# Optimization experiments

Measured on AMD Instinct MI355X. Metric: run time of the kernel, lower is better.

The kernel has to match this reference:

```python
import jax, jax.numpy as jnp
import numpy as np

H, B, N, D, VD, FFH = 8, 16, 512, 512, 64, 2048
NPICK = N // 2
NORM = 1.0 / np.sqrt(VD)


def _ha_encoder(h, W_query, W_key, W_val, W1, W2, W3, W4, W5, W6):
    # h: [B, N, D]; weights: [H, D, VD]
    np_ = NPICK
    pick, dlv = h[:, :np_], h[:, np_:]
    proj = lambda x, W: jnp.einsum('bnd,hdk->hbnk', x, W)
    Q, K, V = proj(h, W_query), proj(h, W_key), proj(h, W_val)
    Kp, Kd = K[:, :, :np_], K[:, :, np_:]   # shared projections (same W_key)
    Vp, Vd = V[:, :, :np_], V[:, :, np_:]
    Qp = proj(pick, W1); Qpap = proj(pick, W2); Qpad = proj(pick, W3)
    Qd = proj(dlv, W4);  Qdad = proj(dlv, W5);  Qdap = proj(dlv, W6)
    c_main = NORM * jnp.einsum('hbnk,hbmk->hbnm', Q, K)          # [H,B,N,N]
    c_pd = NORM * jnp.sum(Qp * Kd, -1)                           # [H,B,np] paired pick->delivery
    c_pap = NORM * jnp.einsum('hbnk,hbmk->hbnm', Qpap, Kp)       # pick -> all pick
    c_pad = NORM * jnp.einsum('hbnk,hbmk->hbnm', Qpad, Kd)       # pick -> all delivery
    c_dp = NORM * jnp.sum(Qd * Kp, -1)                           # paired delivery->pick
    c_dad = NORM * jnp.einsum('hbnk,hbmk->hbnm', Qdad, Kd)       # delivery -> all delivery
    c_dap = NORM * jnp.einsum('hbnk,hbmk->hbnm', Qdap, Kp)       # delivery -> all pick
    ninf1 = jnp.full((H, h.shape[0], np_), -jnp.inf, c_main.dtype)
    ninf2 = jnp.full((H, h.shape[0], np_, np_), -jnp.inf, c_main.dtype)
    col_pd = jnp.concatenate([c_pd, ninf1], 2)[..., None]        # [H,B,N,1]
    blk_pap = jnp.concatenate([c_pap, ninf2], 2)                 # [H,B,N,np]
    blk_pad = jnp.concatenate([c_pad, ninf2], 2)
    col_dp = jnp.concatenate([ninf1, c_dp], 2)[..., None]
    blk_dad = jnp.concatenate([ninf2, c_dad], 2)
    blk_dap = jnp.concatenate([ninf2, c_dap], 2)
    compat = jnp.concatenate([c_main, col_pd, blk_pap, blk_pad, col_dp, blk_dad, blk_dap], -1)
    a = jax.nn.softmax(compat, -1)                               # [H,B,N,N+2+4*np]
    zpad = jnp.zeros_like(Vd)
    V_add_d = jnp.concatenate([Vd, zpad], 2)                     # [H,B,N,VD]
    V_add_p = jnp.concatenate([zpad, Vp], 2)
    av = lambda w, v: jnp.einsum('hbnm,hbmv->hbnv', w, v)
    i = N
    heads = av(a[..., :N], V)
    heads = heads + a[..., i:i + 1] * V_add_d; i += 1
    heads = heads + av(a[..., i:i + np_], Vp); i += np_
    heads = heads + av(a[..., i:i + np_], Vd); i += np_
    heads = heads + a[..., i:i + 1] * V_add_p; i += 1
    heads = heads + av(a[..., i:i + np_], Vd); i += np_
    heads = heads + av(a[..., i:i + np_], Vp)
    return heads.transpose(1, 2, 0, 3).reshape(h.shape[0], N, H * VD)


def _split_heads(x):
    b, n, hd = x.shape
    return x.reshape(b, n, H, hd // H).transpose(0, 2, 1, 3)


def _mha(q, k, v):
    dk = q.shape[-1]
    w = jax.nn.softmax(jnp.einsum('bhnd,bhmd->bhnm', q, k) / np.sqrt(dk), -1)
    o = jnp.einsum('bhnm,bhmd->bhnd', w, v)
    b, hh, n, d = o.shape
    return o.transpose(0, 2, 1, 3).reshape(b, n, hh * d)


def _ff(x, w1, b1, w2, b2, a):
    return x + (jax.nn.relu(x @ w1 + b1) @ w2 + b2) * a


def _forward(x, W_query, W_key, W_val, W1_query, W2_query, W3_query, W4_query, W5_query, W6_query,
             Wq_w, Wk_w, Wv_w, Wq2p_w, Wq2d_w, Wk2_w, Wv2_w,
             comb_w, comb_b, comb2_w, comb2_b, comb3_w, comb3_b,
             alpha1, alpha2, alpha3,
             ff1_w1, ff1_b1, ff1_w2, ff1_b2, ffa1,
             ff2_w1, ff2_b1, ff2_w2, ff2_b2, ffa2,
             ff3_w1, ff3_b1, ff3_w2, ff3_b2, ffa3):
    # stage 1: heterogeneous attention block (combine_3 / AN3 / FF3)
    ha = _ha_encoder(x, W_query, W_key, W_val, W1_query, W2_query, W3_query, W4_query, W5_query, W6_query)
    out = x + (ha @ comb3_w + comb3_b) * alpha3
    out = _ff(out, ff3_w1, ff3_b1, ff3_w2, ff3_b2, ffa3)
    # stage 2: standard multi-head self-attention (combine / AN1 / FF1)
    q = _split_heads(out @ Wq_w); k = _split_heads(out @ Wk_w); v = _split_heads(out @ Wv_w)
    out = out + (_mha(q, k, v) @ comb_w + comb_b) * alpha1
    out = _ff(out, ff1_w1, ff1_b1, ff1_w2, ff1_b2, ffa1)
    # stage 3: pickup/delivery specific queries (combine_2 / AN2 / FF2)
    q2 = jnp.concatenate([out[:, :NPICK] @ Wq2p_w, out[:, NPICK:] @ Wq2d_w], 1)
    q2 = _split_heads(q2); k2 = _split_heads(out @ Wk2_w); v2 = _split_heads(out @ Wv2_w)
    out = out + (_mha(q2, k2, v2) @ comb2_w + comb2_b) * alpha2
    out = _ff(out, ff2_w1, ff2_b1, ff2_w2, ff2_b2, ffa2)
    return out


def setup_inputs() -> dict:
    key = jax.random.key(0)
    ks = jax.random.split(key, 64)
    it = iter(range(64))
    def nrm(shape):
        return jax.random.normal(ks[next(it)], shape, jnp.float32)
    def uni(shape):
        s = 1.0 / np.sqrt(shape[-1])  # torch init_parameters: uniform(-1/sqrt(size(-1)), ...)
        return jax.random.uniform(ks[next(it)], shape, jnp.float32, -s, s)
    d = {'x': nrm((B, N, D))}
    for n in ['W_query', 'W_key', 'W_val', 'W1_query', 'W2_query', 'W3_query', 'W4_query', 'W5_query', 'W6_query']:
        d[n] = uni((H, D, VD))
    for n in ['Wq_w', 'Wk_w', 'Wv_w', 'Wq2p_w', 'Wq2d_w', 'Wk2_w', 'Wv2_w']:
        d[n] = uni((D, H * VD))
    for n in ['comb_w', 'comb2_w', 'comb3_w']:
        d[n] = uni((H * VD, D))
    for n in ['comb_b', 'comb2_b', 'comb3_b']:
        d[n] = uni((D,))
    for n in ['alpha1', 'alpha2', 'alpha3']:
        d[n] = uni((1,))
    for i in ['1', '2', '3']:
        d['ff' + i + '_w1'] = uni((D, FFH))
        d['ff' + i + '_b1'] = uni((FFH,))
        d['ff' + i + '_w2'] = uni((FFH, D))
        d['ff' + i + '_b2'] = uni((D,))
        d['ffa' + i] = uni((1,))
    return d


def reference(x, W_query, W_key, W_val, W1_query, W2_query, W3_query, W4_query, W5_query, W6_query,
              Wq_w, Wk_w, Wv_w, Wq2p_w, Wq2d_w, Wk2_w, Wv2_w,
              comb_w, comb_b, comb2_w, comb2_b, comb3_w, comb3_b,
              alpha1, alpha2, alpha3,
              ff1_w1, ff1_b1, ff1_w2, ff1_b2, ffa1,
              ff2_w1, ff2_b1, ff2_w2, ff2_b2, ffa2,
              ff3_w1, ff3_b1, ff3_w2, ff3_b2, ffa3):
    return _forward(x, W_query, W_key, W_val, W1_query, W2_query, W3_query, W4_query, W5_query, W6_query,
                    Wq_w, Wk_w, Wv_w, Wq2p_w, Wq2d_w, Wk2_w, Wv2_w,
                    comb_w, comb_b, comb2_w, comb2_b, comb3_w, comb3_b,
                    alpha1, alpha2, alpha3,
                    ff1_w1, ff1_b1, ff1_w2, ff1_b2, ffa1,
                    ff2_w1, ff2_b1, ff2_w2, ff2_b2, ffa2,
                    ff3_w1, ff3_b1, ff3_w2, ff3_b2, ffa3)
```

## Files before the change

kernel.cpp:

```cpp
#include <hip/hip_runtime.h>
#include <math.h>

#define Hh 8
#define Bb 16
#define Nn 512
#define Dd 512
#define VDd 64
#define NPICKk 256
#define NORMF 0.125f
#define SCL2 0.1803368801f

typedef unsigned short ushortT;
typedef __bf16 bf16x8 __attribute__((ext_vector_type(8)));
typedef float f32x4 __attribute__((ext_vector_type(4)));

struct PtrsB { const ushortT* p[12]; };
struct PtrsD { ushortT* p[6]; };
struct Ptrs9 { const float* p[9]; };
struct Ptrs10 { const float* p[10]; };
struct Ptrs6 { const float* p[6]; };

__device__ inline ushortT f2bf(float f) {
    __bf16 h = (__bf16)f;
    union { __bf16 h; ushortT u; } v; v.h = h;
    return v.u;
}
__device__ inline float bf2f(ushortT u) {
    union { unsigned int u; float f; } v; v.u = ((unsigned int)u) << 16;
    return v.f;
}
__device__ inline float exp2fast(float x) {
#if __has_builtin(__builtin_amdgcn_exp2f)
    return __builtin_amdgcn_exp2f(x);
#else
    return exp2f(x);
#endif
}
__device__ inline void gload16(const void* gptr, void* ldsptr) {
    auto g = reinterpret_cast<const __attribute__((address_space(1))) unsigned int*>(
        reinterpret_cast<uintptr_t>(gptr));
    auto l = reinterpret_cast<__attribute__((address_space(3))) unsigned int*>(
        reinterpret_cast<uintptr_t>(ldsptr));
    __builtin_amdgcn_global_load_lds(g, l, 16, 0, 0);
}

#define LIX(r, g) (((r) << 6) + ((((g) ^ ((r) & 7))) << 3))

__global__ __launch_bounds__(256) void castx(const float* __restrict__ in,
                                             ushortT* __restrict__ out) {
    int i = blockIdx.x * 256 + threadIdx.x;
    float4 v = *(const float4*)&in[(size_t)i * 4];
    ushort4 o; o.x = f2bf(v.x); o.y = f2bf(v.y); o.z = f2bf(v.z); o.w = f2bf(v.w);
    *(ushort4*)&out[(size_t)i * 4] = o;
}

__device__ inline void tbody(const float* __restrict__ in, ushortT* __restrict__ out,
                             int in_ld, int out_ld, int r0, int c0) {
    __shared__ float T[64][65];
    int tr = threadIdx.x >> 4, tc4 = (threadIdx.x & 15) * 4;
#pragma unroll
    for (int p = 0; p < 4; ++p) {
        float4 v = *(const float4*)&in[(size_t)(r0 + tr + p * 16) * in_ld + c0 + tc4];
        T[tr + p * 16][tc4 + 0] = v.x; T[tr + p * 16][tc4 + 1] = v.y;
        T[tr + p * 16][tc4 + 2] = v.z; T[tr + p * 16][tc4 + 3] = v.w;
    }
    __syncthreads();
#pragma unroll
    for (int p = 0; p < 4; ++p) {
        int orow = c0 + tr + p * 16;
        int ocol = r0 + tc4;
        ushort4 o;
        o.x = f2bf(T[tc4 + 0][tr + p * 16]);
        o.y = f2bf(T[tc4 + 1][tr + p * 16]);
        o.z = f2bf(T[tc4 + 2][tr + p * 16]);
        o.w = f2bf(T[tc4 + 3][tr + p * 16]);
        *(ushort4*)&out[(size_t)orow * out_ld + ocol] = o;
    }
}

__global__ __launch_bounds__(256) void thead(Ptrs9 s, ushortT* __restrict__ dst) {
    int w = blockIdx.z >> 3, h = blockIdx.z & 7;
    tbody(s.p[w] + (size_t)h * 512 * 64,
          dst + (size_t)w * 262144 + (size_t)h * 64 * 512,
          64, 512, blockIdx.y * 64, 0);
}
__global__ __launch_bounds__(256) void tsq(Ptrs10 s, ushortT* __restrict__ dst) {
    tbody(s.p[blockIdx.z], dst + (size_t)blockIdx.z * 262144,
          512, 512, blockIdx.y * 64, blockIdx.x * 64);
}
__global__ __launch_bounds__(256) void tff(Ptrs6 s, ushortT* __restrict__ dst) {
    int z = blockIdx.z;
    if (z < 3) { if (blockIdx.y >= 8 || blockIdx.x >= 32) return; }
    else       { if (blockIdx.y >= 32 || blockIdx.x >= 8) return; }
    int in_ld = (z < 3) ? 2048 : 512;
    int out_ld = (z < 3) ? 512 : 2048;
    tbody(s.p[z], dst + (size_t)z * 1048576, in_ld, out_ld,
          blockIdx.y * 64, blockIdx.x * 64);
}

__global__ __launch_bounds__(256) void gemm_bf(
    PtrsB Bp, PtrsD Db, const ushortT* __restrict__ A, float* __restrict__ outF,
    int M, int N, int K, const float* __restrict__ bias,
    const float* __restrict__ res, const float* __restrict__ alpha,
    int do_relu, int nroute, int vtmask, int scmask)
{
    __shared__ __align__(16) ushortT As[128 * 64];
    __shared__ __align__(16) ushortT Bs[128 * 64];
    const int tid = threadIdx.x;
    const int wid = tid >> 6, lane = tid & 63;
    const int wm = wid >> 1, wn = wid & 1;
    const int l15 = lane & 15, l4 = lane >> 4;

    int bid = blockIdx.y * gridDim.x + blockIdx.x;
    int nwg = gridDim.x * gridDim.y;
    int q = nwg >> 3;
    int swz = (bid & 7) * q + (bid >> 3);
    int bx = swz % gridDim.x, by = swz / gridDim.x;

    const int r0 = by * 128, c0 = bx * 128;
    const int half = ((r0 & (Nn - 1)) >= NPICKk) ? 1 : 0;
    const ushortT* Bt = Bp.p[((c0 >> 9) << 1) | half];
    const int cB = nroute ? (c0 & 511) : c0;

    const ushortT* aSrc[4];
    const ushortT* bSrc[4];
    char* ldsA[4];
    char* ldsB[4];
#pragma unroll
    for (int i = 0; i < 4; ++i) {
        int off = wid * 4096 + i * 1024 + lane * 16;
        int row = off >> 7;
        int sg = ((off >> 4) & 7) ^ (row & 7);
        aSrc[i] = A + (size_t)(r0 + row) * K + sg * 8;
        bSrc[i] = Bt + (size_t)(cB + row) * K + sg * 8;
        ldsA[i] = (char*)As + off;
        ldsB[i] = (char*)Bs + off;
    }

    f32x4 acc[4][4] = {};

    for (int kt = 0; kt < K; kt += 64) {
        __syncthreads();
#pragma unroll
        for (int i = 0; i < 4; ++i) {
            gload16(aSrc[i] + kt, ldsA[i]);
            gload16(bSrc[i] + kt, ldsB[i]);
        }
        asm volatile("s_waitcnt vmcnt(0)" ::: "memory");
        __syncthreads();
#pragma unroll
        for (int kk = 0; kk < 2; ++kk) {
            int g0 = kk * 4 + l4;
            bf16x8 af[4], bfv[4];
#pragma unroll
            for (int mi = 0; mi < 4; ++mi)
                af[mi] = *(const bf16x8*)&As[LIX(wm * 64 + mi * 16 + l15, g0)];
#pragma unroll
            for (int ni = 0; ni < 4; ++ni)
                bfv[ni] = *(const bf16x8*)&Bs[LIX(wn * 64 + ni * 16 + l15, g0)];
#pragma unroll
            for (int mi = 0; mi < 4; ++mi)
#pragma unroll
                for (int ni = 0; ni < 4; ++ni)
                    acc[mi][ni] = __builtin_amdgcn_mfma_f32_16x16x32_bf16(
                        bfv[ni], af[mi], acc[mi][ni], 0, 0, 0);
        }
    }

    if (nroute) {
#pragma unroll
        for (int mi = 0; mi < 4; ++mi) {
            int row = r0 + wm * 64 + mi * 16 + l15;
#pragma unroll
            for (int ni = 0; ni < 4; ++ni) {
                int col = c0 + wn * 64 + ni * 16 + l4 * 4;
                int range = col >> 9, cc = col & 511;
                ushortT* d = Db.p[range];
                f32x4 a = acc[mi][ni];
                if ((scmask >> range) & 1) {
                    a[0] *= SCL2; a[1] *= SCL2; a[2] *= SCL2; a[3] *= SCL2;
                }
                if ((vtmask >> range) & 1) {
                    size_t vb = ((size_t)(row >> 9) * Hh + (cc >> 6)) * 64 + (cc & 63);
                    int tok = row & 511;
#pragma unroll
                    for (int r = 0; r < 4; ++r)
                        d[((vb + r) << 9) + tok] = f2bf(a[r]);
                } else {
                    ushort4 o;
                    o.x = f2bf(a[0]); o.y = f2bf(a[1]);
                    o.z = f2bf(a[2]); o.w = f2bf(a[3]);
                    *(ushort4*)&d[((size_t)row << 9) + cc] = o;
                }
            }
        }
    } else {
        const float alp = alpha ? alpha[0] : 1.0f;
        ushortT* outB = Db.p[0];
#pragma unroll
        for (int mi = 0; mi < 4; ++mi) {
            int row = r0 + wm * 64 + mi * 16 + l15;
#pragma unroll
            for (int ni = 0; ni < 4; ++ni) {
                int colb = c0 + wn * 64 + ni * 16 + l4 * 4;
                f32x4 a = acc[mi][ni];
                if (bias) {
                    float4 b4 = *(const float4*)&bias[colb];
                    a[0] += b4.x; a[1] += b4.y; a[2] += b4.z; a[3] += b4.w;
                }
                if (do_relu) {
#pragma unroll
                    for (int r = 0; r < 4; ++r) a[r] = fmaxf(a[r], 0.f);
                }
#pragma unroll
                for (int r = 0; r < 4; ++r) a[r] *= alp;
                size_t idx = (size_t)row * N + colb;
                if (res) {
                    float4 r4 = *(const float4*)&res[idx];
                    a[0] += r4.x; a[1] += r4.y; a[2] += r4.z; a[3] += r4.w;
                }
                if (outF)
                    *(float4*)&outF[idx] = make_float4(a[0], a[1], a[2], a[3]);
                if (outB) {
                    ushort4 o;
                    o.x = f2bf(a[0]); o.y = f2bf(a[1]);
                    o.z = f2bf(a[2]); o.w = f2bf(a[3]);
                    *(ushort4*)&outB[idx] = o;
                }
            }
        }
    }
}

__global__ __launch_bounds__(256) void gemm64(
    const ushortT* __restrict__ Bw, const ushortT* __restrict__ A,
    float* __restrict__ outF, ushortT* __restrict__ outB,
    int M, int N, int K, const float* __restrict__ bias,
    const float* __restrict__ resf, const ushortT* __restrict__ resb,
    const float* __restrict__ alpha, int do_relu)
{
    __shared__ __align__(16) ushortT As[64 * 64];
    __shared__ __align__(16) ushortT Bs[128 * 64];
    const int tid = threadIdx.x;
    const int wid = tid >> 6, lane = tid & 63;
    const int wm = wid >> 1, wn = wid & 1;
    const int l15 = lane & 15, l4 = lane >> 4;

    int bid = blockIdx.y * gridDim.x + blockIdx.x;
    int nwg = gridDim.x * gridDim.y;
    int q = nwg >> 3;
    int swz = (bid & 7) * q + (bid >> 3);
    int bx = swz % gridDim.x, by = swz / gridDim.x;
    const int r0 = by * 64, c0 = bx * 128;

    const ushortT* aSrc[2];
    char* ldsA[2];
#pragma unroll
    for (int i = 0; i < 2; ++i) {
        int off = wid * 2048 + i * 1024 + lane * 16;
        int row = off >> 7;
        int sg = ((off >> 4) & 7) ^ (row & 7);
        aSrc[i] = A + (size_t)(r0 + row) * K + sg * 8;
        ldsA[i] = (char*)As + off;
    }
    const ushortT* bSrc[4];
    char* ldsB[4];
#pragma unroll
    for (int i = 0; i < 4; ++i) {
        int off = wid * 4096 + i * 1024 + lane * 16;
        int row = off >> 7;
        int sg = ((off >> 4) & 7) ^ (row & 7);
        bSrc[i] = Bw + (size_t)(c0 + row) * K + sg * 8;
        ldsB[i] = (char*)Bs + off;
    }

    f32x4 acc[2][4] = {};

    for (int kt = 0; kt < K; kt += 64) {
        __syncthreads();
#pragma unroll
        for (int i = 0; i < 2; ++i) gload16(aSrc[i] + kt, ldsA[i]);
#pragma unroll
        for (int i = 0; i < 4; ++i) gload16(bSrc[i] + kt, ldsB[i]);
        asm volatile("s_waitcnt vmcnt(0)" ::: "memory");
        __syncthreads();
#pragma unroll
        for (int kk = 0; kk < 2; ++kk) {
            int g0 = kk * 4 + l4;
            bf16x8 af[2], bfv[4];
#pragma unroll
            for (int mi = 0; mi < 2; ++mi)
                af[mi] = *(const bf16x8*)&As[LIX(wm * 32 + mi * 16 + l15, g0)];
#pragma unroll
            for (int ni = 0; ni < 4; ++ni)
                bfv[ni] = *(const bf16x8*)&Bs[LIX(wn * 64 + ni * 16 + l15, g0)];
#pragma unroll
            for (int mi = 0; mi < 2; ++mi)
#pragma unroll
                for (int ni = 0; ni < 4; ++ni)
                    acc[mi][ni] = __builtin_amdgcn_mfma_f32_16x16x32_bf16(
                        bfv[ni], af[mi], acc[mi][ni], 0, 0, 0);
        }
    }

    const float alp = alpha ? alpha[0] : 1.0f;
#pragma unroll
    for (int mi = 0; mi < 2; ++mi) {
        int row = r0 + wm * 32 + mi * 16 + l15;
#pragma unroll
        for (int ni = 0; ni < 4; ++ni) {
            int colb = c0 + wn * 64 + ni * 16 + l4 * 4;
            f32x4 a = acc[mi][ni];
            if (bias) {
                float4 b4 = *(const float4*)&bias[colb];
                a[0] += b4.x; a[1] += b4.y; a[2] += b4.z; a[3] += b4.w;
            }
            if (do_relu) {
#pragma unroll
                for (int r = 0; r < 4; ++r) a[r] = fmaxf(a[r], 0.f);
            }
#pragma unroll
            for (int r = 0; r < 4; ++r) a[r] *= alp;
            size_t idx = (size_t)row * N + colb;
            if (resf) {
                float4 r4 = *(const float4*)&resf[idx];
                a[0] += r4.x; a[1] += r4.y; a[2] += r4.z; a[3] += r4.w;
            }
            if (resb) {
                ushort4 r4 = *(const ushort4*)&resb[idx];
                a[0] += bf2f(r4.x); a[1] += bf2f(r4.y);
                a[2] += bf2f(r4.z); a[3] += bf2f(r4.w);
            }
            if (outF)
                *(float4*)&outF[idx] = make_float4(a[0], a[1], a[2], a[3]);
            if (outB) {
                ushort4 o;
                o.x = f2bf(a[0]); o.y = f2bf(a[1]);
                o.z = f2bf(a[2]); o.w = f2bf(a[3]);
                *(ushort4*)&outB[idx] = o;
            }
        }
    }
}

__global__ __launch_bounds__(256) void diag_dot_bb(const ushortT* __restrict__ QD,
                                                   const ushortT* __restrict__ K,
                                                   float* __restrict__ Sdg) {
    int i = blockIdx.x * 256 + threadIdx.x;
    int h = i & 7, n = (i >> 3) & 511, b = i >> 12;
    int dix = (n < NPICKk) ? n + NPICKk : n - NPICKk;
    const ushortT* q = QD + (((size_t)(b * Nn + n) * Hh + h) << 6);
    const ushortT* k = K + (((size_t)(b * Nn + dix) * Hh + h) << 6);
    float s = 0.f;
#pragma unroll
    for (int d = 0; d < 64; d += 4) {
        ushort4 a = *(const ushort4*)(q + d);
        ushort4 c = *(const ushort4*)(k + d);
        s += bf2f(a.x) * bf2f(c.x) + bf2f(a.y) * bf2f(c.y)
           + bf2f(a.z) * bf2f(c.z) + bf2f(a.w) * bf2f(c.w);
    }
    Sdg[i] = s;
}

template <int HA>
__global__ __launch_bounds__(256) void attn9(
    const ushortT* __restrict__ Qm, const ushortT* __restrict__ Km,
    const ushortT* __restrict__ Vtm, const ushortT* __restrict__ QAm,
    const ushortT* __restrict__ QBm, const float* __restrict__ Sdg,
    ushortT* __restrict__ Out)
{
    __shared__ __align__(16) ushortT Ks[64 * 64];
    __shared__ __align__(16) ushortT Vs[64 * 64];
    __shared__ __align__(16) ushortT Pw[4][16 * 64];
    __shared__ float sdl[64];

    const int tid = threadIdx.x, wid = tid >> 6, lane = tid & 63;
    const int l15 = lane & 15, l4 = lane >> 4;

    const int p = blockIdx.x + (blockIdx.y << 3) + (blockIdx.z << 6);
    const int n0 = (((p >> 3) & 7)) << 6;
    const int g8 = (p & 7) | ((p >> 6) << 3);
    const int h = g8 & 7, b = g8 >> 3;
    const int bh = b * Hh + h;

    const size_t qrow = (((size_t)(b * Nn + n0 + wid * 16 + l15) * Hh + h) << 6);
    bf16x8 qf[2], xaf[2], xbf[2];
#pragma unroll
    for (int kk = 0; kk < 2; ++kk) {
        int g0 = kk * 4 + l4;
        qf[kk] = *(const bf16x8*)&Qm[qrow + g0 * 8];
        if (HA) {
            xaf[kk] = *(const bf16x8*)&QAm[qrow + g0 * 8];
            xbf[kk] = *(const bf16x8*)&QBm[qrow + g0 * 8];
        }
    }
    if (HA && tid < 64) sdl[tid] = Sdg[((size_t)(b * Nn + n0 + tid)) * Hh + h];
    const int td = (n0 < NPICKk) ? ((n0 + NPICKk) >> 6) : ((n0 - NPICKk) >> 6);

    const ushortT* kSrc[2]; char* kDst[2];
    const ushortT* vSrc[2]; char* vDst[2];
#pragma unroll
    for (int i = 0; i < 2; ++i) {
        int off = wid * 2048 + i * 1024 + lane * 16;
        int row = off >> 7, sg = ((off >> 4) & 7) ^ (row & 7);
        kSrc[i] = Km + (((size_t)(b * Nn + row) * Hh + h) << 6) + sg * 8;
        kDst[i] = (char*)Ks + off;
        vSrc[i] = Vtm + (((size_t)(bh * 64 + row)) << 9) + sg * 8;
        vDst[i] = (char*)Vs + off;
    }

    float M[4], L[4];
    f32x4 Oa[4] = {};
#pragma unroll
    for (int r = 0; r < 4; ++r) { M[r] = -INFINITY; L[r] = 0.f; }

    for (int t = 0; t < 8; ++t) {
        __syncthreads();
#pragma unroll
        for (int i = 0; i < 2; ++i) {
            gload16(kSrc[i] + (size_t)t * (64 * Hh * VDd), kDst[i]);
            gload16(vSrc[i] + t * 64, vDst[i]);
        }
        asm volatile("s_waitcnt vmcnt(0)" ::: "memory");
        __syncthreads();

        __builtin_amdgcn_s_setprio(1);
        f32x4 s1[4] = {}, sX[4] = {};
#pragma unroll
        for (int kk = 0; kk < 2; ++kk) {
            bf16x8 aq = qf[kk];
            bf16x8 ax;
            if (HA) ax = (t >= 4) ? xbf[kk] : xaf[kk];
#pragma unroll
            for (int ni = 0; ni < 4; ++ni) {
                bf16x8 bk = *(const bf16x8*)&Ks[LIX(ni * 16 + l15, kk * 4 + l4)];
                s1[ni] = __builtin_amdgcn_mfma_f32_16x16x32_bf16(aq, bk, s1[ni], 0, 0, 0);
                if (HA)
                    sX[ni] = __builtin_amdgcn_mfma_f32_16x16x32_bf16(ax, bk, sX[ni], 0, 0, 0);
            }
        }
        __builtin_amdgcn_s_setprio(0);

        const bool dt = HA && (t == td);

        float mrow[4];
        bool need = false;
#pragma unroll
        for (int r = 0; r < 4; ++r) {
            int rw = wid * 16 + l4 * 4 + r;
            float m = s1[0][r];
#pragma unroll
            for (int ni = 1; ni < 4; ++ni) m = fmaxf(m, s1[ni][r]);
            if (HA) {
#pragma unroll
                for (int ni = 0; ni < 4; ++ni) m = fmaxf(m, sX[ni][r]);
            }
            if (dt) m = fmaxf(m, sdl[rw]);
#pragma unroll
            for (int o = 8; o >= 1; o >>= 1) m = fmaxf(m, __shfl_xor(m, o, 16));
            mrow[r] = m;
            need = need || (m > M[r] + 8.f);
        }
        if (__any(need)) {
#pragma unroll
            for (int r = 0; r < 4; ++r) {
                float mn = fmaxf(M[r], mrow[r]);
                float sc = exp2fast(M[r] - mn);
                M[r] = mn; L[r] *= sc;
#pragma unroll
                for (int ni = 0; ni < 4; ++ni) Oa[ni][r] *= sc;
            }
        }

#pragma unroll
        for (int r = 0; r < 4; ++r) {
            int rw = wid * 16 + l4 * 4 + r;
            float rs = 0.f;
#pragma unroll
            for (int ni = 0; ni < 4; ++ni) {
                float pv = exp2fast(s1[ni][r] - M[r]);
                if (HA) pv += exp2fast(sX[ni][r] - M[r]);
                if (dt && ni == wid && l15 == l4 * 4 + r) pv += exp2fast(sdl[rw] - M[r]);
                s1[ni][r] = pv;
                rs += pv;
            }
#pragma unroll
            for (int o = 8; o >= 1; o >>= 1) rs += __shfl_xor(rs, o, 16);
            L[r] += rs;
        }

#pragma unroll
        for (int ni = 0; ni < 4; ++ni)
#pragma unroll
            for (int r = 0; r < 4; ++r) {
                int prow = l4 * 4 + r;
                int col = ni * 16 + l15;
                Pw[wid][(prow << 6) + ((((col >> 3) ^ (prow & 7))) << 3) + (col & 7)] =
                    f2bf(s1[ni][r]);
            }

        __builtin_amdgcn_s_setprio(1);
#pragma unroll
        for (int kk = 0; kk < 2; ++kk) {
            int g0 = kk * 4 + l4;
            bf16x8 ap = *(const bf16x8*)&Pw[wid][LIX(l15, g0)];
#pragma unroll
            for (int ni = 0; ni < 4; ++ni) {
                bf16x8 bv = *(const bf16x8*)&Vs[LIX(ni * 16 + l15, g0)];
                Oa[ni] = __builtin_amdgcn_mfma_f32_16x16x32_bf16(ap, bv, Oa[ni], 0, 0, 0);
            }
        }
        __builtin_amdgcn_s_setprio(0);
    }

#pragma unroll
    for (int r = 0; r < 4; ++r) {
        float inv = 1.0f / L[r];
        size_t obase = (((size_t)(b * Nn + n0 + wid * 16 + l4 * 4 + r) * Hh + h) << 6);
#pragma unroll
        for (int ni = 0; ni < 4; ++ni)
            Out[obase + ni * 16 + l15] = f2bf(Oa[ni][r] * inv);
    }
}

extern "C" void kernel_launch(void* const* d_in, const int* in_sizes, int n_in,
                              void* d_out, int out_size, void* d_ws, size_t ws_size,
                              hipStream_t stream)
{
    const float* x = (const float*)d_in[0];

    int dictOrder = (in_sizes[18] != 512);
    const float* comb_w  = (const float*)d_in[17];
    const float* comb2_w = (const float*)d_in[dictOrder ? 18 : 19];
    const float* comb3_w = (const float*)d_in[dictOrder ? 19 : 21];
    const float* comb_b  = (const float*)d_in[dictOrder ? 20 : 18];
    const float* comb2_b = (const float*)d_in[dictOrder ? 21 : 20];
    const float* comb3_b = (const float*)d_in[22];
    const float* alpha1 = (const float*)d_in[23];
    const float* alpha2 = (const float*)d_in[24];
    const float* alpha3 = (const float*)d_in[25];
    const float* ff1_w1 = (const float*)d_in[26];
    const float* ff1_b1 = (const float*)d_in[27];
    const float* ff1_w2 = (const float*)d_in[28];
    const float* ff1_b2 = (const float*)d_in[29];
    const float* ffa1   = (const float*)d_in[30];
    const float* ff2_w1 = (const float*)d_in[31];
    const float* ff2_b1 = (const float*)d_in[32];
    const float* ff2_w2 = (const float*)d_in[33];
    const float* ff2_b2 = (const float*)d_in[34];
    const float* ffa2   = (const float*)d_in[35];
    const float* ff3_w1 = (const float*)d_in[36];
    const float* ff3_b1 = (const float*)d_in[37];
    const float* ff3_w2 = (const float*)d_in[38];
    const float* ff3_b2 = (const float*)d_in[39];
    const float* ffa3   = (const float*)d_in[40];

    char* W = (char*)d_ws;
    ushortT* wbHead = (ushortT*)(W + 0);
    ushortT* wbMha  = (ushortT*)(W + 4718592);
    ushortT* wbComb = (ushortT*)(W + 8388608);
    ushortT* wbFf1  = (ushortT*)(W + 9961472);
    ushortT* wbFf2  = (ushortT*)(W + 16252928);
    ushortT* xbf    = (ushortT*)(W + 22544384);
    float*   Sd     = (float*)  (W + 30932992);
    ushortT* bufQ   = (ushortT*)(W + 31195136);
    ushortT* bufK   = (ushortT*)(W + 39583744);
    ushortT* bufVt  = (ushortT*)(W + 47972352);
    ushortT* bufQA  = (ushortT*)(W + 56360960);
    ushortT* bufQB  = (ushortT*)(W + 64749568);
    ushortT* bufQD  = (ushortT*)(W + 73138176);
    ushortT* hidden = (ushortT*)(W + 81526784);
    ushortT* curb   = (ushortT*)(W + 115081216);
    ushortT* bufHA  = xbf;
    float*   cur    = (float*)d_out;

    dim3 tb(256);
    const int TOK = Bb * Nn;
    const size_t WS = 512 * 512;
    const size_t WF = 2048 * 512;

    hipLaunchKernelGGL(castx, dim3(TOK * 512 / 1024), tb, 0, stream, x, xbf);
    {
        Ptrs9 s; for (int i = 0; i < 9; ++i) s.p[i] = (const float*)d_in[1 + i];
        hipLaunchKernelGGL(thead, dim3(1, 8, 72), tb, 0, stream, s, wbHead);
    }
    {
        Ptrs10 s;
        for (int i = 0; i < 7; ++i) s.p[i] = (const float*)d_in[10 + i];
        s.p[7] = comb_w; s.p[8] = comb2_w; s.p[9] = comb3_w;
        hipLaunchKernelGGL(tsq, dim3(8, 8, 10), tb, 0, stream, s, wbMha);
    }
    {
        Ptrs6 s;
        s.p[0] = ff1_w1; s.p[1] = ff2_w1; s.p[2] = ff3_w1;
        s.p[3] = ff1_w2; s.p[4] = ff2_w2; s.p[5] = ff3_w2;
        hipLaunchKernelGGL(tff, dim3(32, 32, 6), tb, 0, stream, s, wbFf1);
    }

    auto gemm = [&](PtrsB Bp, PtrsD Db, const ushortT* A, float* oF,
                    int M, int Ncc, int Kc, const float* bias, const float* res,
                    const float* alp, int relu, int nroute, int vtmask, int scmask) {
        hipLaunchKernelGGL(gemm_bf, dim3(Ncc / 128, M / 128), tb, 0, stream,
                           Bp, Db, A, oF, M, Ncc, Kc, bias, res, alp, relu, nroute,
                           vtmask, scmask);
    };
    auto g64 = [&](const ushortT* Bw, const ushortT* A, float* oF, ushortT* oB,
                   int M, int Ncc, int Kc, const float* bias, const float* resf,
                   const ushortT* resb, const float* alp, int relu) {
        hipLaunchKernelGGL(gemm64, dim3(Ncc / 128, M / 64), tb, 0, stream,
                           Bw, A, oF, oB, M, Ncc, Kc, bias, resf, resb, alp, relu);
    };
    auto uni = [&](const ushortT* w) { PtrsB b; for (int i = 0; i < 12; ++i) b.p[i] = w; return b; };
    auto d1 = [&](ushortT* d) { PtrsD dd = {}; dd.p[0] = d; return dd; };

    {
        PtrsB b;
        b.p[0] = b.p[1] = wbHead + 0 * WS;
        b.p[2] = b.p[3] = wbHead + 1 * WS;
        b.p[4] = b.p[5] = wbHead + 2 * WS;
        b.p[6] = wbHead + 4 * WS; b.p[7] = wbHead + 8 * WS;
        b.p[8] = wbHead + 5 * WS; b.p[9] = wbHead + 7 * WS;
        b.p[10] = wbHead + 3 * WS; b.p[11] = wbHead + 6 * WS;
        PtrsD d; d.p[0] = bufQ; d.p[1] = bufK; d.p[2] = bufVt;
        d.p[3] = bufQA; d.p[4] = bufQB; d.p[5] = bufQD;
        gemm(b, d, xbf, nullptr, TOK, 3072, 512, nullptr, nullptr, nullptr, 0, 6, 4, 57);
    }

    hipLaunchKernelGGL(diag_dot_bb, dim3(Bb * Nn * Hh / 256), tb, 0, stream, bufQD, bufK, Sd);
    hipLaunchKernelGGL((attn9<1>), dim3(Nn / 64, Hh, Bb), tb, 0, stream,
                       bufQ, bufK, bufVt, bufQA, bufQB, Sd, bufHA);

    g64(wbComb + 2 * WS, bufHA, nullptr, curb, TOK, 512, 512, comb3_b, x, nullptr, alpha3, 0);
    gemm(uni(wbFf1 + 2 * WF), d1(hidden), curb, nullptr, TOK, 2048, 512, ff3_b1, nullptr, nullptr, 1, 0, 0, 0);
    g64(wbFf2 + 2 * WF, hidden, nullptr, curb, TOK, 512, 2048, ff3_b2, nullptr, curb, ffa3, 0);

    {
        PtrsB b;
        b.p[0] = b.p[1] = wbMha + 0 * WS;
        b.p[2] = b.p[3] = wbMha + 1 * WS;
        b.p[4] = b.p[5] = wbMha + 2 * WS;
        PtrsD d = {}; d.p[0] = bufQ; d.p[1] = bufK; d.p[2] = bufVt;
        gemm(b, d, curb, nullptr, TOK, 1536, 512, nullptr, nullptr, nullptr, 0, 3, 4, 1);
    }
    hipLaunchKernelGGL((attn9<0>), dim3(Nn / 64, Hh, Bb), tb, 0, stream,
                       bufQ, bufK, bufVt, nullptr, nullptr, nullptr, bufHA);
    g64(wbComb + 0 * WS, bufHA, nullptr, curb, TOK, 512, 512, comb_b, nullptr, curb, alpha1, 0);
    gemm(uni(wbFf1 + 0 * WF), d1(hidden), curb, nullptr, TOK, 2048, 512, ff1_b1, nullptr, nullptr, 1, 0, 0, 0);
    g64(wbFf2 + 0 * WF, hidden, nullptr, curb, TOK, 512, 2048, ff1_b2, nullptr, curb, ffa1, 0);

    {
        PtrsB b;
        b.p[0] = wbMha + 3 * WS; b.p[1] = wbMha + 4 * WS;
        b.p[2] = b.p[3] = wbMha + 5 * WS;
        b.p[4] = b.p[5] = wbMha + 6 * WS;
        PtrsD d = {}; d.p[0] = bufQ; d.p[1] = bufK; d.p[2] = bufVt;
        gemm(b, d, curb, nullptr, TOK, 1536, 512, nullptr, nullptr, nullptr, 0, 3, 4, 1);
    }
    hipLaunchKernelGGL((attn9<0>), dim3(Nn / 64, Hh, Bb), tb, 0, stream,
                       bufQ, bufK, bufVt, nullptr, nullptr, nullptr, bufHA);
    g64(wbComb + 1 * WS, bufHA, nullptr, curb, TOK, 512, 512, comb2_b, nullptr, curb, alpha2, 0);
    gemm(uni(wbFf1 + 1 * WF), d1(hidden), curb, nullptr, TOK, 2048, 512, ff2_b1, nullptr, nullptr, 1, 0, 0, 0);
    g64(wbFf2 + 1 * WF, hidden, cur, nullptr, TOK, 512, 2048, ff2_b2, nullptr, curb, ffa2, 0);
}
```

Measured before the change: 502.4 us.

## Register-prefetch next K/V tile in attention and defer row-sum reduction

The attention kernel now loads the next K/V tile from global memory into registers while the current tile is computed, then stores it to shared memory at the top of the next iteration, replacing synchronous direct-to-LDS loads with a full vmcnt wait. The per-tile max shuffle reduction is moved inside the rare rescale branch, and the row-sum shuffle reduction is deferred to the epilogue using per-lane partial sums. Both aim to hide global load latency and cut cross-lane shuffles per tile. The cost is more registers for the prefetch buffers, which may reduce occupancy. The skip test for rescaling now compares per-lane maxima instead of the reduced row maximum.

```diff
diff --git a/kernel.cpp b/kernel.cpp
--- a/kernel.cpp
+++ b/kernel.cpp
@@ -363,7 +363,7 @@
 }
 
 template <int HA>
-__global__ __launch_bounds__(256) void attn9(
+__global__ __launch_bounds__(256) void attn10(
     const ushortT* __restrict__ Qm, const ushortT* __restrict__ Km,
     const ushortT* __restrict__ Vtm, const ushortT* __restrict__ QAm,
     const ushortT* __restrict__ QBm, const float* __restrict__ Sdg,
@@ -397,32 +397,49 @@
     if (HA && tid < 64) sdl[tid] = Sdg[((size_t)(b * Nn + n0 + tid)) * Hh + h];
     const int td = (n0 < NPICKk) ? ((n0 + NPICKk) >> 6) : ((n0 - NPICKk) >> 6);
 
-    const ushortT* kSrc[2]; char* kDst[2];
-    const ushortT* vSrc[2]; char* vDst[2];
+    const ushortT* kSrc[2]; ushortT* kDst[2];
+    const ushortT* vSrc[2]; ushortT* vDst[2];
 #pragma unroll
     for (int i = 0; i < 2; ++i) {
         int off = wid * 2048 + i * 1024 + lane * 16;
         int row = off >> 7, sg = ((off >> 4) & 7) ^ (row & 7);
         kSrc[i] = Km + (((size_t)(b * Nn + row) * Hh + h) << 6) + sg * 8;
-        kDst[i] = (char*)Ks + off;
+        kDst[i] = (ushortT*)((char*)Ks + off);
         vSrc[i] = Vtm + (((size_t)(bh * 64 + row)) << 9) + sg * 8;
-        vDst[i] = (char*)Vs + off;
-    }
-
-    float M[4], L[4];
+        vDst[i] = (ushortT*)((char*)Vs + off);
+    }
+
+    float M[4], Lp[4];
     f32x4 Oa[4] = {};
 #pragma unroll
-    for (int r = 0; r < 4; ++r) { M[r] = -INFINITY; L[r] = 0.f; }
-
+    for (int r = 0; r < 4; ++r) { M[r] = -INFINITY; Lp[r] = 0.f; }
+
+    bf16x8 krbuf[2][2], vrbuf[2][2];
+#pragma unroll
+    for (int i = 0; i < 2; ++i) {
+        krbuf[0][i] = *(const bf16x8*)kSrc[i];
+        vrbuf[0][i] = *(const bf16x8*)vSrc[i];
+    }
+
+#pragma unroll
     for (int t = 0; t < 8; ++t) {
-        __syncthreads();
+        const int cur = t & 1, nxt = cur ^ 1;
+        __builtin_amdgcn_s_barrier();
 #pragma unroll
         for (int i = 0; i < 2; ++i) {
-            gload16(kSrc[i] + (size_t)t * (64 * Hh * VDd), kDst[i]);
-            gload16(vSrc[i] + t * 64, vDst[i]);
-        }
-        asm volatile("s_waitcnt vmcnt(0)" ::: "memory");
-        __syncthreads();
+            *(bf16x8*)kDst[i] = krbuf[cur][i];
+            *(bf16x8*)vDst[i] = vrbuf[cur][i];
+        }
+        if (t < 7) {
+#pragma unroll
+            for (int i = 0; i < 2; ++i) {
+                krbuf[nxt][i] = *(const bf16x8*)(kSrc[i] + (size_t)(t + 1) * (64 * Hh * VDd));
+                vrbuf[nxt][i] = *(const bf16x8*)(vSrc[i] + (t + 1) * 64);
+            }
+        }
+        asm volatile("s_waitcnt lgkmcnt(0)" ::: "memory");
+        __builtin_amdgcn_s_barrier();
+        __builtin_amdgcn_sched_barrier(0);
 
         __builtin_amdgcn_s_setprio(1);
         f32x4 s1[4] = {}, sX[4] = {};
@@ -443,8 +460,8 @@
 
         const bool dt = HA && (t == td);
 
-        float mrow[4];
-        bool need = false;
+        float mloc[4];
+        bool grow = false;
 #pragma unroll
         for (int r = 0; r < 4; ++r) {
             int rw = wid * 16 + l4 * 4 + r;
@@ -455,18 +472,19 @@
 #pragma unroll
                 for (int ni = 0; ni < 4; ++ni) m = fmaxf(m, sX[ni][r]);
             }
-            if (dt) m = fmaxf(m, sdl[rw]);
-#pragma unroll
-            for (int o = 8; o >= 1; o >>= 1) m = fmaxf(m, __shfl_xor(m, o, 16));
-            mrow[r] = m;
-            need = need || (m > M[r] + 8.f);
-        }
-        if (__any(need)) {
+            if (dt && l15 == l4 * 4 + r) m = fmaxf(m, sdl[rw]);
+            mloc[r] = m;
+            grow = grow || (m > M[r] + 8.f);
+        }
+        if (__any(grow)) {
 #pragma unroll
             for (int r = 0; r < 4; ++r) {
-                float mn = fmaxf(M[r], mrow[r]);
+                float m = mloc[r];
+#pragma unroll
+                for (int o = 8; o >= 1; o >>= 1) m = fmaxf(m, __shfl_xor(m, o, 16));
+                float mn = fmaxf(M[r], m);
                 float sc = exp2fast(M[r] - mn);
-                M[r] = mn; L[r] *= sc;
+                M[r] = mn; Lp[r] *= sc;
 #pragma unroll
                 for (int ni = 0; ni < 4; ++ni) Oa[ni][r] *= sc;
             }
@@ -484,9 +502,7 @@
                 s1[ni][r] = pv;
                 rs += pv;
             }
-#pragma unroll
-            for (int o = 8; o >= 1; o >>= 1) rs += __shfl_xor(rs, o, 16);
-            L[r] += rs;
+            Lp[r] += rs;
         }
 
 #pragma unroll
@@ -515,7 +531,10 @@
 
 #pragma unroll
     for (int r = 0; r < 4; ++r) {
-        float inv = 1.0f / L[r];
+        float l = Lp[r];
+#pragma unroll
+        for (int o = 8; o >= 1; o >>= 1) l += __shfl_xor(l, o, 16);
+        float inv = 1.0f / l;
         size_t obase = (((size_t)(b * Nn + n0 + wid * 16 + l4 * 4 + r) * Hh + h) << 6);
 #pragma unroll
         for (int ni = 0; ni < 4; ++ni)
@@ -627,7 +646,7 @@
     }
 
     hipLaunchKernelGGL(diag_dot_bb, dim3(Bb * Nn * Hh / 256), tb, 0, stream, bufQD, bufK, Sd);
-    hipLaunchKernelGGL((attn9<1>), dim3(Nn / 64, Hh, Bb), tb, 0, stream,
+    hipLaunchKernelGGL((attn10<1>), dim3(Nn / 64, Hh, Bb), tb, 0, stream,
                        bufQ, bufK, bufVt, bufQA, bufQB, Sd, bufHA);
 
     g64(wbComb + 2 * WS, bufHA, nullptr, curb, TOK, 512, 512, comb3_b, x, nullptr, alpha3, 0);
@@ -642,7 +661,7 @@
         PtrsD d = {}; d.p[0] = bufQ; d.p[1] = bufK; d.p[2] = bufVt;
         gemm(b, d, curb, nullptr, TOK, 1536, 512, nullptr, nullptr, nullptr, 0, 3, 4, 1);
     }
-    hipLaunchKernelGGL((attn9<0>), dim3(Nn / 64, Hh, Bb), tb, 0, stream,
+    hipLaunchKernelGGL((attn10<0>), dim3(Nn / 64, Hh, Bb), tb, 0, stream,
                        bufQ, bufK, bufVt, nullptr, nullptr, nullptr, bufHA);
     g64(wbComb + 0 * WS, bufHA, nullptr, curb, TOK, 512, 512, comb_b, nullptr, curb, alpha1, 0);
     gemm(uni(wbFf1 + 0 * WF), d1(hidden), curb, nullptr, TOK, 2048, 512, ff1_b1, nullptr, nullptr, 1, 0, 0, 0);
@@ -656,7 +675,7 @@
         PtrsD d = {}; d.p[0] = bufQ; d.p[1] = bufK; d.p[2] = bufVt;
         gemm(b, d, curb, nullptr, TOK, 1536, 512, nullptr, nullptr, nullptr, 0, 3, 4, 1);
     }
-    hipLaunchKernelGGL((attn9<0>), dim3(Nn / 64, Hh, Bb), tb, 0, stream,
+    hipLaunchKernelGGL((attn10<0>), dim3(Nn / 64, Hh, Bb), tb, 0, stream,
                        bufQ, bufK, bufVt, nullptr, nullptr, nullptr, bufHA);
     g64(wbComb + 1 * WS, bufHA, nullptr, curb, TOK, 512, 512, comb2_b, nullptr, curb, alpha2, 0);
     gemm(uni(wbFf1 + 1 * WF), d1(hidden), curb, nullptr, TOK, 2048, 512, ff2_b1, nullptr, nullptr, 1, 0, 0, 0);
```

Result: faster. 474.9 us (-5.5%).
